# Kernel optimization log

Hardware: AMD Instinct MI355X
Metric: run time of the kernel (lower is better)

Reference implementation:

```python
import jax, jax.numpy as jnp
import numpy as np

DIM = 192
STATE = 64
B = 8
H = 64
W = 64
EPS_LN = 1e-5
EPS_BN = 1e-5


def _layernorm(x, g, b):
    m = jnp.mean(x, axis=-1, keepdims=True)
    v = jnp.mean((x - m) ** 2, axis=-1, keepdims=True)
    return (x - m) / jnp.sqrt(v + EPS_LN) * g + b


def _linear(x, w, b=None):
    # torch Linear convention: w is [out, in]
    y = jnp.einsum('...i,oi->...o', x, w)
    return y if b is None else y + b


def _parallel_scan(A, Bd, xp):
    # A, Bd, xp: [B, L, S]; h_t = A_t*h_{t-1} + Bd_t*xp_t via log-space cumsum
    A_safe = jnp.clip(A, 0.001, 0.999)
    log_A = jnp.log(A_safe + 1e-10)
    log_cum_A = jnp.cumsum(log_A, axis=1)
    log_cum_A_max = jnp.max(log_cum_A, axis=1, keepdims=True)
    cum_A = jnp.exp(log_cum_A - log_cum_A_max)
    BX = Bd * xp
    # prepend zeros, drop last: normalizer uses cumprod up to t-1
    log_pad = jnp.pad(log_cum_A - log_cum_A_max, ((0, 0), (1, 0), (0, 0)))[:, :-1]
    BX_norm = BX * jnp.exp(-log_pad)
    return jnp.cumsum(BX_norm, axis=1) * cum_A


def _ssm(x, ln_g, ln_b, xp_w, xp_b, dt_w, dt_b, A_log, B_w, C_w, Dp, out_w, out_b):
    xn = _layernorm(x, ln_g, ln_b)
    delta = jax.nn.softplus(_linear(xn, dt_w, dt_b)) * 0.01 + 0.0001  # [B,L,S]
    B_t = _linear(xn, B_w)
    C_t = _linear(xn, C_w)
    A = -jnp.exp(A_log)  # [S]
    x_proj = _linear(xn, xp_w, xp_b)
    deltaA = jnp.clip(delta * A, -10.0, -0.0001)
    A_disc = jnp.exp(deltaA)
    B_disc = delta * B_t
    h = _parallel_scan(A_disc, B_disc, x_proj)
    y = C_t * h
    y = jnp.where(jnp.all(jnp.isfinite(y)), y, jnp.zeros_like(y))
    y = _linear(y, out_w, out_b)
    return y + jnp.clip(Dp, -2.0, 2.0) * x


def reference(x, ln1_g, ln1_b, ln2_g, ln2_b, dw_w, bn_g, bn_b, bn_rm, bn_rv,
              ssm_ln_g, ssm_ln_b, xp_w, xp_b, dt_w, dt_b, A_log, B_w, C_w,
              D_param, out_w, out_b, mlp_w1, mlp_b1, mlp_w2, mlp_b2,
              alpha_local, alpha_ssm, alpha_mlp):
    identity = x
    # depthwise 3x3 conv + BatchNorm2d (eval mode, running stats)
    xc = jax.lax.conv_general_dilated(
        x, dw_w, (1, 1), 'SAME', feature_group_count=DIM,
        dimension_numbers=('NCHW', 'OIHW', 'NCHW'))
    scale = (bn_g / jnp.sqrt(bn_rv + EPS_BN))[None, :, None, None]
    x_local = (xc - bn_rm[None, :, None, None]) * scale + bn_b[None, :, None, None]
    # SSM branch on flattened spatial sequence
    x_seq = x.transpose(0, 2, 3, 1).reshape(B, H * W, DIM)
    x_seq = _layernorm(x_seq, ln1_g, ln1_b)
    x_seq = _ssm(x_seq, ssm_ln_g, ssm_ln_b, xp_w, xp_b, dt_w, dt_b, A_log,
                 B_w, C_w, D_param, out_w, out_b)
    x_ssm = x_seq.reshape(B, H, W, DIM).transpose(0, 3, 1, 2)
    xr = identity + alpha_local * x_local + alpha_ssm * x_ssm
    # residual MLP (dropout = identity at inference)
    x_mlp = xr.transpose(0, 2, 3, 1).reshape(B, H * W, DIM)
    x_mlp = _layernorm(x_mlp, ln2_g, ln2_b)
    x_mlp = _linear(jax.nn.gelu(_linear(x_mlp, mlp_w1, mlp_b1), approximate=False),
                    mlp_w2, mlp_b2)
    return xr + alpha_mlp * x_mlp.reshape(B, H, W, DIM).transpose(0, 3, 1, 2)


def setup_inputs() -> dict:
    key = jax.random.key(0)
    ks = jax.random.split(key, 12)
    def nrm(k, shape, s):
        return jax.random.normal(k, shape, jnp.float32) * s
    f32 = jnp.float32
    return {
        'x': jax.random.normal(ks[0], (B, DIM, H, W), f32),
        'ln1_g': jnp.ones(DIM, f32), 'ln1_b': jnp.zeros(DIM, f32),
        'ln2_g': jnp.ones(DIM, f32), 'ln2_b': jnp.zeros(DIM, f32),
        'dw_w': nrm(ks[1], (DIM, 1, 3, 3), 0.2),
        'bn_g': jnp.ones(DIM, f32), 'bn_b': jnp.zeros(DIM, f32),
        'bn_rm': jnp.zeros(DIM, f32), 'bn_rv': jnp.ones(DIM, f32),
        'ssm_ln_g': jnp.ones(DIM, f32), 'ssm_ln_b': jnp.zeros(DIM, f32),
        'xp_w': nrm(ks[2], (STATE, DIM), 0.05), 'xp_b': jnp.zeros(STATE, f32),
        'dt_w': nrm(ks[3], (STATE, DIM), 0.05), 'dt_b': jnp.zeros(STATE, f32),
        'A_log': jnp.log(jax.random.uniform(ks[4], (STATE,), f32) * 0.8 + 0.2),
        'B_w': nrm(ks[5], (STATE, DIM), 0.05),
        'C_w': nrm(ks[6], (STATE, DIM), 0.05),
        'D_param': jnp.zeros(DIM, f32),
        'out_w': nrm(ks[7], (DIM, STATE), 0.05), 'out_b': jnp.zeros(DIM, f32),
        'mlp_w1': nrm(ks[8], (4 * DIM, DIM), 0.03), 'mlp_b1': jnp.zeros(4 * DIM, f32),
        'mlp_w2': nrm(ks[9], (DIM, 4 * DIM), 0.03), 'mlp_b2': jnp.zeros(DIM, f32),
        'alpha_local': jnp.full((1,), 0.5, f32),
        'alpha_ssm': jnp.full((1,), 0.5, f32),
        'alpha_mlp': jnp.full((1,), 0.5, f32),
    }
```

## Files before the change

kernel.cpp:

```cpp
#include <hip/hip_runtime.h>
#include <hip/hip_bf16.h>
#include <math.h>


#define DEV static __device__ __forceinline__

constexpr int Bn = 8, Dm = 192, Ln = 4096, Sn = 64, Hd = 768;

typedef __attribute__((ext_vector_type(8))) short bf16x8;
typedef __attribute__((ext_vector_type(4))) float f32x4;

DEV float wave_sum(float v) {
#pragma unroll
  for (int off = 1; off < 64; off <<= 1) v += __shfl_xor(v, off);
  return v;
}

DEV short f2b(float x) {
  __hip_bfloat16 h = __float2bfloat16(x);
  return *(short*)&h;
}

DEV float b2f(short x) {
  __hip_bfloat16 h = *(__hip_bfloat16*)&x;
  return __bfloat162float(h);
}

__global__ __launch_bounds__(256) void k_ln(
    const float* __restrict__ x, const float* __restrict__ g1, const float* __restrict__ b1,
    const float* __restrict__ g2, const float* __restrict__ b2,
    short* __restrict__ xnb, short* __restrict__ xln1b) {
  __shared__ __align__(16) float tile[Dm * 65];
  int b = blockIdx.y, l0 = blockIdx.x * 64, tid = threadIdx.x;
  const float* xb = x + (size_t)b * Dm * Ln;
  for (int i = tid; i < Dm * 16; i += 256) {
    int d = i >> 4, l4 = (i & 15) << 2;
    float4 v = *(const float4*)&xb[d * Ln + l0 + l4];
    tile[d * 65 + l4]     = v.x; tile[d * 65 + l4 + 1] = v.y;
    tile[d * 65 + l4 + 2] = v.z; tile[d * 65 + l4 + 3] = v.w;
  }
  __syncthreads();
  int lane = tid & 63, wv = tid >> 6;
  float ga0 = g1[lane], ga1 = g1[lane + 64], ga2 = g1[lane + 128];
  float bb0 = b1[lane], bb1 = b1[lane + 64], bb2 = b1[lane + 128];
  float gc0 = g2[lane], gc1 = g2[lane + 64], gc2 = g2[lane + 128];
  float bc0 = b2[lane], bc1 = b2[lane + 64], bc2 = b2[lane + 128];
  for (int li = wv; li < 64; li += 4) {
    float v0 = tile[lane * 65 + li], v1 = tile[(lane + 64) * 65 + li], v2 = tile[(lane + 128) * 65 + li];
    float s  = wave_sum(v0 + v1 + v2);
    float sq = wave_sum(v0 * v0 + v1 * v1 + v2 * v2);
    float m = s * (1.f / 192.f);
    float inv = rsqrtf(sq * (1.f / 192.f) - m * m + 1e-5f);
    float y0 = (v0 - m) * inv * ga0 + bb0;
    float y1 = (v1 - m) * inv * ga1 + bb1;
    float y2 = (v2 - m) * inv * ga2 + bb2;
    float s2  = wave_sum(y0 + y1 + y2);
    float sq2 = wave_sum(y0 * y0 + y1 * y1 + y2 * y2);
    float m2 = s2 * (1.f / 192.f);
    float inv2 = rsqrtf(sq2 * (1.f / 192.f) - m2 * m2 + 1e-5f);
    size_t base = ((size_t)b * Ln + l0 + li) * Dm;
    xln1b[base + lane]       = f2b(y0);
    xln1b[base + lane + 64]  = f2b(y1);
    xln1b[base + lane + 128] = f2b(y2);
    xnb[base + lane]       = f2b((y0 - m2) * inv2 * gc0 + bc0);
    xnb[base + lane + 64]  = f2b((y1 - m2) * inv2 * gc1 + bc1);
    xnb[base + lane + 128] = f2b((y2 - m2) * inv2 * gc2 + bc2);
  }
}

__global__ __launch_bounds__(256) void k_wconv(
    const float* __restrict__ dt_w, const float* __restrict__ B_w,
    const float* __restrict__ C_w, const float* __restrict__ xp_w,
    const float* __restrict__ out_w, const float* __restrict__ w1,
    const float* __restrict__ w2, short* __restrict__ wb) {
  int i = blockIdx.x * 256 + threadIdx.x;
  const float4* src;
  if (i < 3072)       src = (const float4*)dt_w + i;
  else if (i < 6144)  src = (const float4*)B_w + (i - 3072);
  else if (i < 9216)  src = (const float4*)C_w + (i - 6144);
  else if (i < 12288) src = (const float4*)xp_w + (i - 9216);
  else if (i < 15360) src = (const float4*)out_w + (i - 12288);
  else if (i < 52224) src = (const float4*)w1 + (i - 15360);
  else                src = (const float4*)w2 + (i - 52224);
  float4 v = *src;
  int o = i * 4;
  wb[o]     = f2b(v.x); wb[o + 1] = f2b(v.y);
  wb[o + 2] = f2b(v.z); wb[o + 3] = f2b(v.w);
}

__global__ __launch_bounds__(256) void k_proj(
    const short* __restrict__ xnb, const short* __restrict__ wcat,
    const float* __restrict__ dt_b, const float* __restrict__ xp_b,
    const float* __restrict__ A_log, float* __restrict__ abc) {
  __shared__ __align__(16) short As[64 * 72];
  __shared__ __align__(16) short Bs[256 * 72];
  int m0 = blockIdx.x * 64, tid = threadIdx.x;
  int lane = tid & 63, l16 = lane & 15, quad = lane >> 4, w = tid >> 6;
  f32x4 acc[16] = {};
  for (int kt = 0; kt < 3; kt++) {
    int kb = kt * 64;
    for (int i = tid; i < 512; i += 256) {
      int row = i >> 3, c8 = (i & 7) * 8;
      *(float4*)&As[row * 72 + c8] = *(const float4*)&xnb[(size_t)(m0 + row) * 192 + kb + c8];
    }
    for (int i = tid; i < 2048; i += 256) {
      int row = i >> 3, c8 = (i & 7) * 8;
      *(float4*)&Bs[row * 72 + c8] = *(const float4*)&wcat[(size_t)row * 192 + kb + c8];
    }
    __syncthreads();
#pragma unroll
    for (int ks = 0; ks < 2; ks++) {
      int ko = ks * 32 + quad * 8;
      bf16x8 a0 = *(const bf16x8*)&As[(w * 16 + l16) * 72 + ko];
#pragma unroll
      for (int nh = 0; nh < 2; nh++) {
        bf16x8 bfr[8];
#pragma unroll
        for (int j = 0; j < 8; j++) bfr[j] = *(const bf16x8*)&Bs[((nh * 8 + j) * 16 + l16) * 72 + ko];
#pragma unroll
        for (int j = 0; j < 8; j++)
          acc[nh * 8 + j] = __builtin_amdgcn_mfma_f32_16x16x32_bf16(a0, bfr[j], acc[nh * 8 + j], 0, 0, 0);
      }
    }
    __syncthreads();
  }
  float Av[4], dtb[4], xpb[4];
#pragma unroll
  for (int ni = 0; ni < 4; ni++) {
    int s = ni * 16 + l16;
    Av[ni] = -expf(A_log[s]); dtb[ni] = dt_b[s]; xpb[ni] = xp_b[s];
  }
#pragma unroll
  for (int r = 0; r < 4; r++) {
    int m = m0 + w * 16 + quad * 4 + r;
    float* orow = abc + (size_t)m * 192;
#pragma unroll
    for (int ni = 0; ni < 4; ni++) {
      int s = ni * 16 + l16;
      float z = acc[ni][r] + dtb[ni];
      float sp = (z > 20.f) ? z : log1pf(expf(z));
      float delta = sp * 0.01f + 0.0001f;
      float bt  = acc[ni + 4][r];
      float ct  = acc[ni + 8][r];
      float xpv = acc[ni + 12][r] + xpb[ni];
      float dA = fminf(fmaxf(delta * Av[ni], -10.f), -0.0001f);
      float Ae = fminf(fmaxf(expf(dA), 0.001f), 0.999f) + 1e-10f;
      orow[s]       = Ae;
      orow[64 + s]  = delta * bt * xpv;
      orow[128 + s] = ct;
    }
  }
}

__global__ __launch_bounds__(64) void k_scan1(const float* __restrict__ abc, float* __restrict__ sums) {
  int c = blockIdx.x, b = blockIdx.y, s = threadIdx.x;
  const float* p = abc + ((size_t)b * Ln + c * 32) * 192;
  float prodA = 1.f, h = 0.f;
  int t = 0;
  if (c == 0) { prodA = p[s]; h = p[64 + s]; t = 1; }
#pragma unroll 4
  for (; t < 32; t++) {
    float a = p[t * 192 + s], bx = p[t * 192 + 64 + s];
    h = a * (h + bx);
    prodA *= a;
  }
  int ci = b * 128 + c;
  sums[(ci * 2 + 0) * 64 + s] = prodA;
  sums[(ci * 2 + 1) * 64 + s] = h;
}

__global__ __launch_bounds__(64) void k_scan2(const float* __restrict__ sums, float* __restrict__ carries) {
  int b = blockIdx.x, s = threadIdx.x;
  float cur = 0.f;
#pragma unroll 4
  for (int c = 0; c < 128; c++) {
    int ci = b * 128 + c;
    carries[ci * 64 + s] = cur;
    cur = sums[(ci * 2 + 0) * 64 + s] * cur + sums[(ci * 2 + 1) * 64 + s];
  }
}

__global__ __launch_bounds__(64) void k_scan3(const float* __restrict__ abc, const float* __restrict__ carries,
                                              short* __restrict__ y) {
  int c = blockIdx.x, b = blockIdx.y, s = threadIdx.x;
  size_t r0 = (size_t)b * Ln + c * 32;
  const float* p = abc + r0 * 192;
  short* yo = y + r0 * 64;
  float h = carries[(b * 128 + c) * 64 + s];
  int t = 0;
  if (c == 0) { h = p[64 + s]; yo[s] = f2b(p[128 + s] * h); t = 1; }
#pragma unroll 4
  for (; t < 32; t++) {
    float a = p[t * 192 + s], bx = p[t * 192 + 64 + s], ct = p[t * 192 + 128 + s];
    h = a * (h + bx);
    yo[t * 64 + s] = f2b(ct * h);
  }
}

__global__ __launch_bounds__(256) void k_out(
    const short* __restrict__ y, const short* __restrict__ owb, const float* __restrict__ out_b,
    const float* __restrict__ Dp, const short* __restrict__ xln1b, float* __restrict__ sout) {
  __shared__ __align__(16) short As[96 * 72];
  __shared__ __align__(16) short Bs[64 * 72];
  int l0g = blockIdx.x * 64, d0 = blockIdx.y * 96, tid = threadIdx.x;
  int lane = tid & 63, l16 = lane & 15, quad = lane >> 4;
  int wm = (tid >> 6) >> 1, wn = (tid >> 6) & 1;
  f32x4 acc[3][2] = {};
  for (int i = tid; i < 768; i += 256) {
    int row = i >> 3, c8 = (i & 7) * 8;
    *(float4*)&As[row * 72 + c8] = *(const float4*)&owb[(d0 + row) * 64 + c8];
  }
  for (int i = tid; i < 512; i += 256) {
    int row = i >> 3, c8 = (i & 7) * 8;
    *(float4*)&Bs[row * 72 + c8] = *(const float4*)&y[(size_t)(l0g + row) * 64 + c8];
  }
  __syncthreads();
#pragma unroll
  for (int ks = 0; ks < 2; ks++) {
    int ko = ks * 32 + quad * 8;
    bf16x8 a[3], b[2];
#pragma unroll
    for (int mi = 0; mi < 3; mi++) a[mi] = *(const bf16x8*)&As[(wm * 48 + mi * 16 + l16) * 72 + ko];
#pragma unroll
    for (int ni = 0; ni < 2; ni++) b[ni] = *(const bf16x8*)&Bs[(wn * 32 + ni * 16 + l16) * 72 + ko];
#pragma unroll
    for (int mi = 0; mi < 3; mi++)
#pragma unroll
      for (int ni = 0; ni < 2; ni++)
        acc[mi][ni] = __builtin_amdgcn_mfma_f32_16x16x32_bf16(a[mi], b[ni], acc[mi][ni], 0, 0, 0);
  }
  int bb = l0g >> 12;
#pragma unroll
  for (int mi = 0; mi < 3; mi++)
#pragma unroll
    for (int r = 0; r < 4; r++) {
      int d = d0 + wm * 48 + mi * 16 + quad * 4 + r;
      float ob = out_b[d];
      float dc = fminf(fmaxf(Dp[d], -2.f), 2.f);
#pragma unroll
      for (int ni = 0; ni < 2; ni++) {
        int l = l0g + wn * 32 + ni * 16 + l16;
        float v = acc[mi][ni][r] + ob;
        if (dc != 0.f) v += dc * b2f(xln1b[(size_t)l * 192 + d]);
        sout[((size_t)bb * Dm + d) * Ln + (l & 4095)] = v;
      }
    }
}

__global__ __launch_bounds__(256) void k_conv(
    const float* __restrict__ x, const float* __restrict__ dw,
    const float* __restrict__ bn_g, const float* __restrict__ bn_b,
    const float* __restrict__ bn_rm, const float* __restrict__ bn_rv,
    const float* __restrict__ sout, const float* __restrict__ a_loc,
    const float* __restrict__ a_ssm, float* __restrict__ xr) {
  __shared__ __align__(16) float xs[64 * 64];
  int d = blockIdx.x, b = blockIdx.y, tid = threadIdx.x;
  const float* xp = x + ((size_t)b * Dm + d) * Ln;
  for (int i = tid; i < 1024; i += 256) ((float4*)xs)[i] = ((const float4*)xp)[i];
  __syncthreads();
  float w[9];
#pragma unroll
  for (int k = 0; k < 9; k++) w[k] = dw[d * 9 + k];
  float scale = bn_g[d] * rsqrtf(bn_rv[d] + 1e-5f);
  float rm = bn_rm[d], bb = bn_b[d];
  float al = a_loc[0], as_ = a_ssm[0];
  const float* sp = sout + ((size_t)b * Dm + d) * Ln;
  float* xo = xr + ((size_t)b * Dm + d) * Ln;
  for (int i = tid; i < 4096; i += 256) {
    int h = i >> 6, wc = i & 63;
    float acc = 0.f;
#pragma unroll
    for (int kh = 0; kh < 3; kh++) {
      int hh = h + kh - 1;
      if (hh < 0 || hh >= 64) continue;
#pragma unroll
      for (int kw = 0; kw < 3; kw++) {
        int ww2 = wc + kw - 1;
        if (ww2 < 0 || ww2 >= 64) continue;
        acc += xs[hh * 64 + ww2] * w[kh * 3 + kw];
      }
    }
    float xl = (acc - rm) * scale + bb;
    xo[i] = xs[i] + al * xl + as_ * sp[i];
  }
}

__global__ __launch_bounds__(256) void k_ln2(
    const float* __restrict__ xr, const float* __restrict__ g, const float* __restrict__ bb,
    short* __restrict__ xn2) {
  __shared__ __align__(16) float tile[Dm * 65];
  int b = blockIdx.y, l0 = blockIdx.x * 64, tid = threadIdx.x;
  const float* xb = xr + (size_t)b * Dm * Ln;
  for (int i = tid; i < Dm * 16; i += 256) {
    int d = i >> 4, l4 = (i & 15) << 2;
    float4 v = *(const float4*)&xb[d * Ln + l0 + l4];
    tile[d * 65 + l4]     = v.x; tile[d * 65 + l4 + 1] = v.y;
    tile[d * 65 + l4 + 2] = v.z; tile[d * 65 + l4 + 3] = v.w;
  }
  __syncthreads();
  int lane = tid & 63, wv = tid >> 6;
  float g0 = g[lane], g1v = g[lane + 64], g2v = g[lane + 128];
  float b0 = bb[lane], b1v = bb[lane + 64], b2v = bb[lane + 128];
  for (int li = wv; li < 64; li += 4) {
    float v0 = tile[lane * 65 + li], v1 = tile[(lane + 64) * 65 + li], v2 = tile[(lane + 128) * 65 + li];
    float s  = wave_sum(v0 + v1 + v2);
    float sq = wave_sum(v0 * v0 + v1 * v1 + v2 * v2);
    float m = s * (1.f / 192.f);
    float inv = rsqrtf(sq * (1.f / 192.f) - m * m + 1e-5f);
    size_t base = ((size_t)b * Ln + l0 + li) * Dm;
    xn2[base + lane]       = f2b((v0 - m) * inv * g0 + b0);
    xn2[base + lane + 64]  = f2b((v1 - m) * inv * g1v + b1v);
    xn2[base + lane + 128] = f2b((v2 - m) * inv * g2v + b2v);
  }
}

__global__ __launch_bounds__(256) void k_gemm1(
    const short* __restrict__ xn2, const short* __restrict__ w1b,
    const float* __restrict__ b1h, short* __restrict__ hid) {
  __shared__ __align__(16) short smem[2 * 128 * 88];
  short* As = smem;
  short* Bs = smem + 128 * 88;
  int m0 = blockIdx.x * 128, n0 = blockIdx.y * 128, tid = threadIdx.x;
  int lane = tid & 63, l16 = lane & 15, quad = lane >> 4;
  int wm = (tid >> 6) >> 1, wn = (tid >> 6) & 1;
  f32x4 acc[4][4] = {};
  for (int kt = 0; kt < 3; kt++) {
    int kb = kt * 64;
    for (int i = tid; i < 1024; i += 256) {
      int row = i >> 3, c8 = (i & 7) * 8;
      *(float4*)&As[row * 88 + c8] = *(const float4*)&xn2[(size_t)(m0 + row) * 192 + kb + c8];
      *(float4*)&Bs[row * 88 + c8] = *(const float4*)&w1b[(size_t)(n0 + row) * 192 + kb + c8];
    }
    __syncthreads();
#pragma unroll
    for (int ks = 0; ks < 2; ks++) {
      int ko = ks * 32 + quad * 8;
      bf16x8 a[4], b[4];
#pragma unroll
      for (int mi = 0; mi < 4; mi++) a[mi] = *(const bf16x8*)&As[(wm * 64 + mi * 16 + l16) * 88 + ko];
#pragma unroll
      for (int ni = 0; ni < 4; ni++) b[ni] = *(const bf16x8*)&Bs[(wn * 64 + ni * 16 + l16) * 88 + ko];
#pragma unroll
      for (int mi = 0; mi < 4; mi++)
#pragma unroll
        for (int ni = 0; ni < 4; ni++)
          acc[mi][ni] = __builtin_amdgcn_mfma_f32_16x16x32_bf16(a[mi], b[ni], acc[mi][ni], 0, 0, 0);
    }
    __syncthreads();
  }
  short* Cs = smem;
  float bias4[4];
#pragma unroll
  for (int ni = 0; ni < 4; ni++) bias4[ni] = b1h[n0 + wn * 64 + ni * 16 + l16];
#pragma unroll
  for (int mi = 0; mi < 4; mi++)
#pragma unroll
    for (int ni = 0; ni < 4; ni++) {
      int n = wn * 64 + ni * 16 + l16;
#pragma unroll
      for (int r = 0; r < 4; r++) {
        int m = wm * 64 + mi * 16 + quad * 4 + r;
        float v = acc[mi][ni][r] + bias4[ni];
        float g = 0.5f * v * (1.f + erff(v * 0.70710678118f));
        Cs[m * 136 + n] = f2b(g);
      }
    }
  __syncthreads();
  for (int i = tid; i < 2048; i += 256) {
    int m = i >> 4, ch = i & 15;
    *(float4*)&hid[(size_t)(m0 + m) * 768 + n0 + ch * 8] = *(const float4*)&Cs[m * 136 + ch * 8];
  }
}

__global__ __launch_bounds__(256) void k_gemm2(
    const short* __restrict__ hid, const short* __restrict__ w2b,
    const float* __restrict__ b2o, const float* __restrict__ xr,
    const float* __restrict__ am, float* __restrict__ out) {
  __shared__ __align__(16) short Wt[96 * 88];
  __shared__ __align__(16) short Ht[64 * 88];
  int l0g = blockIdx.x * 64, d0 = blockIdx.y * 96, tid = threadIdx.x;
  int lane = tid & 63, l16 = lane & 15, quad = lane >> 4;
  int wm = (tid >> 6) >> 1, wn = (tid >> 6) & 1;
  f32x4 acc[3][2] = {};
  for (int kt = 0; kt < 12; kt++) {
    int kb = kt * 64;
    for (int i = tid; i < 768; i += 256) {
      int row = i >> 3, c8 = (i & 7) * 8;
      *(float4*)&Wt[row * 88 + c8] = *(const float4*)&w2b[(size_t)(d0 + row) * 768 + kb + c8];
    }
    for (int i = tid; i < 512; i += 256) {
      int row = i >> 3, c8 = (i & 7) * 8;
      *(float4*)&Ht[row * 88 + c8] = *(const float4*)&hid[(size_t)(l0g + row) * 768 + kb + c8];
    }
    __syncthreads();
#pragma unroll
    for (int ks = 0; ks < 2; ks++) {
      int ko = ks * 32 + quad * 8;
      bf16x8 a[3], b[2];
#pragma unroll
      for (int mi = 0; mi < 3; mi++) a[mi] = *(const bf16x8*)&Wt[(wm * 48 + mi * 16 + l16) * 88 + ko];
#pragma unroll
      for (int ni = 0; ni < 2; ni++) b[ni] = *(const bf16x8*)&Ht[(wn * 32 + ni * 16 + l16) * 88 + ko];
#pragma unroll
      for (int mi = 0; mi < 3; mi++)
#pragma unroll
        for (int ni = 0; ni < 2; ni++)
          acc[mi][ni] = __builtin_amdgcn_mfma_f32_16x16x32_bf16(a[mi], b[ni], acc[mi][ni], 0, 0, 0);
    }
    __syncthreads();
  }
  float alpha = am[0];
#pragma unroll
  for (int mi = 0; mi < 3; mi++)
#pragma unroll
    for (int r = 0; r < 4; r++) {
      int d = d0 + wm * 48 + mi * 16 + quad * 4 + r;
      float bias = b2o[d];
#pragma unroll
      for (int ni = 0; ni < 2; ni++) {
        int lg = l0g + wn * 32 + ni * 16 + l16;
        size_t idx = ((size_t)(lg >> 12) * Dm + d) * Ln + (lg & 4095);
        out[idx] = xr[idx] + alpha * (acc[mi][ni][r] + bias);
      }
    }
}

extern "C" void kernel_launch(void* const* d_in, const int* in_sizes, int n_in,
                              void* d_out, int out_size, void* d_ws, size_t ws_size,
                              hipStream_t stream) {
  (void)in_sizes; (void)n_in; (void)out_size; (void)ws_size;
  const float* x     = (const float*)d_in[0];
  const float* ln1_g = (const float*)d_in[1];
  const float* ln1_b = (const float*)d_in[2];
  const float* ln2_g = (const float*)d_in[3];
  const float* ln2_b = (const float*)d_in[4];
  const float* dw_w  = (const float*)d_in[5];
  const float* bn_g  = (const float*)d_in[6];
  const float* bn_b  = (const float*)d_in[7];
  const float* bn_rm = (const float*)d_in[8];
  const float* bn_rv = (const float*)d_in[9];
  const float* ssm_g = (const float*)d_in[10];
  const float* ssm_b = (const float*)d_in[11];
  const float* xp_w  = (const float*)d_in[12];
  const float* xp_b  = (const float*)d_in[13];
  const float* dt_w  = (const float*)d_in[14];
  const float* dt_b  = (const float*)d_in[15];
  const float* A_log = (const float*)d_in[16];
  const float* B_w   = (const float*)d_in[17];
  const float* C_w   = (const float*)d_in[18];
  const float* Dp    = (const float*)d_in[19];
  const float* out_w = (const float*)d_in[20];
  const float* out_b = (const float*)d_in[21];
  const float* w1    = (const float*)d_in[22];
  const float* b1    = (const float*)d_in[23];
  const float* w2    = (const float*)d_in[24];
  const float* b2    = (const float*)d_in[25];
  const float* a_loc = (const float*)d_in[26];
  const float* a_ssm = (const float*)d_in[27];
  const float* a_mlp = (const float*)d_in[28];

  float* ws = (float*)d_ws;
  short* xnb   = (short*)ws;
  short* xln1b = (short*)(ws + 3145728);
  float* abc   = ws + 6291456;
  short* yB    = (short*)(ws + 12582912);
  float* sout  = ws + 13729792;
  float* xr    = ws + 20021248;
  short* wb    = (short*)(ws + 26312704);
  float* sums  = ws + 26490880;
  float* carr  = ws + 26621952;
  short* wcatb = wb;
  short* owb   = wb + 49152;
  short* w1b   = wb + 61440;
  short* w2b   = wb + 208896;
  short* xn2   = (short*)ws;
  short* hid   = (short*)(ws + 6291456);
  float* out   = (float*)d_out;

  k_ln   <<<dim3(64, 8),  256, 0, stream>>>(x, ln1_g, ln1_b, ssm_g, ssm_b, xnb, xln1b);
  k_wconv<<<dim3(348),    256, 0, stream>>>(dt_w, B_w, C_w, xp_w, out_w, w1, w2, wb);
  k_proj <<<dim3(512),    256, 0, stream>>>(xnb, wcatb, dt_b, xp_b, A_log, abc);
  k_scan1<<<dim3(128, 8),  64, 0, stream>>>(abc, sums);
  k_scan2<<<dim3(8),       64, 0, stream>>>(sums, carr);
  k_scan3<<<dim3(128, 8),  64, 0, stream>>>(abc, carr, yB);
  k_out  <<<dim3(512, 2), 256, 0, stream>>>(yB, owb, out_b, Dp, xln1b, sout);
  k_conv <<<dim3(192, 8), 256, 0, stream>>>(x, dw_w, bn_g, bn_b, bn_rm, bn_rv, sout, a_loc, a_ssm, xr);
  k_ln2  <<<dim3(64, 8),  256, 0, stream>>>(xr, ln2_g, ln2_b, xn2);
  k_gemm1<<<dim3(256, 6), 256, 0, stream>>>(xn2, w1b, b1, hid);
  k_gemm2<<<dim3(512, 2), 256, 0, stream>>>(hid, w2b, b2, xr, a_mlp, out);
}
```

Before: 294.8 us.

## Split and compress scan intermediates, halve LN tiles, read activations directly in GEMMs

Measured after the change: 309.1 us. 1.05x slower.

```diff
diff --git a/kernel.cpp b/kernel.cpp
--- a/kernel.cpp
+++ b/kernel.cpp
@@ -30,14 +30,14 @@
     const float* __restrict__ x, const float* __restrict__ g1, const float* __restrict__ b1,
     const float* __restrict__ g2, const float* __restrict__ b2,
     short* __restrict__ xnb, short* __restrict__ xln1b) {
-  __shared__ __align__(16) float tile[Dm * 65];
-  int b = blockIdx.y, l0 = blockIdx.x * 64, tid = threadIdx.x;
+  __shared__ __align__(16) float tile[Dm * 33];
+  int b = blockIdx.y, l0 = blockIdx.x * 32, tid = threadIdx.x;
   const float* xb = x + (size_t)b * Dm * Ln;
-  for (int i = tid; i < Dm * 16; i += 256) {
-    int d = i >> 4, l4 = (i & 15) << 2;
+  for (int i = tid; i < Dm * 8; i += 256) {
+    int d = i >> 3, l4 = (i & 7) << 2;
     float4 v = *(const float4*)&xb[d * Ln + l0 + l4];
-    tile[d * 65 + l4]     = v.x; tile[d * 65 + l4 + 1] = v.y;
-    tile[d * 65 + l4 + 2] = v.z; tile[d * 65 + l4 + 3] = v.w;
+    tile[d * 33 + l4]     = v.x; tile[d * 33 + l4 + 1] = v.y;
+    tile[d * 33 + l4 + 2] = v.z; tile[d * 33 + l4 + 3] = v.w;
   }
   __syncthreads();
   int lane = tid & 63, wv = tid >> 6;
@@ -45,8 +45,8 @@
   float bb0 = b1[lane], bb1 = b1[lane + 64], bb2 = b1[lane + 128];
   float gc0 = g2[lane], gc1 = g2[lane + 64], gc2 = g2[lane + 128];
   float bc0 = b2[lane], bc1 = b2[lane + 64], bc2 = b2[lane + 128];
-  for (int li = wv; li < 64; li += 4) {
-    float v0 = tile[lane * 65 + li], v1 = tile[(lane + 64) * 65 + li], v2 = tile[(lane + 128) * 65 + li];
+  for (int li = wv; li < 32; li += 4) {
+    float v0 = tile[lane * 33 + li], v1 = tile[(lane + 64) * 33 + li], v2 = tile[(lane + 128) * 33 + li];
     float s  = wave_sum(v0 + v1 + v2);
     float sq = wave_sum(v0 * v0 + v1 * v1 + v2 * v2);
     float m = s * (1.f / 192.f);
@@ -74,97 +74,102 @@
     const float* __restrict__ out_w, const float* __restrict__ w1,
     const float* __restrict__ w2, short* __restrict__ wb) {
   int i = blockIdx.x * 256 + threadIdx.x;
+  if (i >= 89088) return;
+  if (i < 12288) {
+    int mat = i / 3072, rem = i % 3072;
+    int s = rem / 48, c4 = rem % 48;
+    const float4* src = (mat == 0) ? (const float4*)dt_w
+                      : (mat == 1) ? (const float4*)B_w
+                      : (mat == 2) ? (const float4*)C_w : (const float4*)xp_w;
+    float4 v = src[rem];
+    int r = (s >> 5) * 128 + (mat * 2 + ((s >> 4) & 1)) * 16 + (s & 15);
+    int o = r * 192 + c4 * 4;
+    wb[o] = f2b(v.x); wb[o + 1] = f2b(v.y); wb[o + 2] = f2b(v.z); wb[o + 3] = f2b(v.w);
+    return;
+  }
   const float4* src;
-  if (i < 3072)       src = (const float4*)dt_w + i;
-  else if (i < 6144)  src = (const float4*)B_w + (i - 3072);
-  else if (i < 9216)  src = (const float4*)C_w + (i - 6144);
-  else if (i < 12288) src = (const float4*)xp_w + (i - 9216);
-  else if (i < 15360) src = (const float4*)out_w + (i - 12288);
+  if (i < 15360)      src = (const float4*)out_w + (i - 12288);
   else if (i < 52224) src = (const float4*)w1 + (i - 15360);
   else                src = (const float4*)w2 + (i - 52224);
   float4 v = *src;
   int o = i * 4;
-  wb[o]     = f2b(v.x); wb[o + 1] = f2b(v.y);
-  wb[o + 2] = f2b(v.z); wb[o + 3] = f2b(v.w);
+  wb[o] = f2b(v.x); wb[o + 1] = f2b(v.y); wb[o + 2] = f2b(v.z); wb[o + 3] = f2b(v.w);
 }
 
 __global__ __launch_bounds__(256) void k_proj(
     const short* __restrict__ xnb, const short* __restrict__ wcat,
     const float* __restrict__ dt_b, const float* __restrict__ xp_b,
-    const float* __restrict__ A_log, float* __restrict__ abc) {
-  __shared__ __align__(16) short As[64 * 72];
+    const float* __restrict__ A_log, float* __restrict__ aA, unsigned* __restrict__ bxc) {
   __shared__ __align__(16) short Bs[256 * 72];
-  int m0 = blockIdx.x * 64, tid = threadIdx.x;
-  int lane = tid & 63, l16 = lane & 15, quad = lane >> 4, w = tid >> 6;
-  f32x4 acc[16] = {};
+  int m0 = blockIdx.x * 32, tid = threadIdx.x;
+  int lane = tid & 63, l16 = lane & 15, quad = lane >> 4;
+  int wm = (tid >> 6) >> 1, wn = (tid >> 6) & 1;
+  f32x4 acc[8] = {};
   for (int kt = 0; kt < 3; kt++) {
     int kb = kt * 64;
-    for (int i = tid; i < 512; i += 256) {
-      int row = i >> 3, c8 = (i & 7) * 8;
-      *(float4*)&As[row * 72 + c8] = *(const float4*)&xnb[(size_t)(m0 + row) * 192 + kb + c8];
-    }
     for (int i = tid; i < 2048; i += 256) {
       int row = i >> 3, c8 = (i & 7) * 8;
-      *(float4*)&Bs[row * 72 + c8] = *(const float4*)&wcat[(size_t)row * 192 + kb + c8];
+      *(float4*)&Bs[row * 72 + c8] = *(const float4*)&wcat[row * 192 + kb + c8];
     }
     __syncthreads();
 #pragma unroll
     for (int ks = 0; ks < 2; ks++) {
       int ko = ks * 32 + quad * 8;
-      bf16x8 a0 = *(const bf16x8*)&As[(w * 16 + l16) * 72 + ko];
-#pragma unroll
-      for (int nh = 0; nh < 2; nh++) {
-        bf16x8 bfr[8];
-#pragma unroll
-        for (int j = 0; j < 8; j++) bfr[j] = *(const bf16x8*)&Bs[((nh * 8 + j) * 16 + l16) * 72 + ko];
-#pragma unroll
-        for (int j = 0; j < 8; j++)
-          acc[nh * 8 + j] = __builtin_amdgcn_mfma_f32_16x16x32_bf16(a0, bfr[j], acc[nh * 8 + j], 0, 0, 0);
+      bf16x8 a0 = *(const bf16x8*)&xnb[(size_t)(m0 + wm * 16 + l16) * 192 + kb + ko];
+#pragma unroll
+      for (int j = 0; j < 8; j++) {
+        bf16x8 bf = *(const bf16x8*)&Bs[(wn * 128 + j * 16 + l16) * 72 + ko];
+        acc[j] = __builtin_amdgcn_mfma_f32_16x16x32_bf16(a0, bf, acc[j], 0, 0, 0);
       }
     }
     __syncthreads();
   }
-  float Av[4], dtb[4], xpb[4];
-#pragma unroll
-  for (int ni = 0; ni < 4; ni++) {
-    int s = ni * 16 + l16;
-    Av[ni] = -expf(A_log[s]); dtb[ni] = dt_b[s]; xpb[ni] = xp_b[s];
+  float Av[2], dtbv[2], xpbv[2];
+#pragma unroll
+  for (int sub = 0; sub < 2; sub++) {
+    int s = wn * 32 + sub * 16 + l16;
+    Av[sub] = -expf(A_log[s]); dtbv[sub] = dt_b[s]; xpbv[sub] = xp_b[s];
   }
 #pragma unroll
   for (int r = 0; r < 4; r++) {
-    int m = m0 + w * 16 + quad * 4 + r;
-    float* orow = abc + (size_t)m * 192;
-#pragma unroll
-    for (int ni = 0; ni < 4; ni++) {
-      int s = ni * 16 + l16;
-      float z = acc[ni][r] + dtb[ni];
+    int m = m0 + wm * 16 + quad * 4 + r;
+#pragma unroll
+    for (int sub = 0; sub < 2; sub++) {
+      int s = wn * 32 + sub * 16 + l16;
+      float z = acc[0 + sub][r] + dtbv[sub];
       float sp = (z > 20.f) ? z : log1pf(expf(z));
       float delta = sp * 0.01f + 0.0001f;
-      float bt  = acc[ni + 4][r];
-      float ct  = acc[ni + 8][r];
-      float xpv = acc[ni + 12][r] + xpb[ni];
-      float dA = fminf(fmaxf(delta * Av[ni], -10.f), -0.0001f);
+      float bt  = acc[2 + sub][r];
+      float ct  = acc[4 + sub][r];
+      float xpv = acc[6 + sub][r] + xpbv[sub];
+      float dA = fminf(fmaxf(delta * Av[sub], -10.f), -0.0001f);
       float Ae = fminf(fmaxf(expf(dA), 0.001f), 0.999f) + 1e-10f;
-      orow[s]       = Ae;
-      orow[64 + s]  = delta * bt * xpv;
-      orow[128 + s] = ct;
-    }
-  }
-}
-
-__global__ __launch_bounds__(64) void k_scan1(const float* __restrict__ abc, float* __restrict__ sums) {
+      aA[(size_t)m * 64 + s] = Ae;
+      unsigned pk = (unsigned)(unsigned short)f2b(delta * bt * xpv)
+                  | ((unsigned)(unsigned short)f2b(ct) << 16);
+      bxc[(size_t)m * 64 + s] = pk;
+    }
+  }
+}
+
+__global__ __launch_bounds__(64) void k_scan1(const float* __restrict__ aA,
+                                              const unsigned* __restrict__ bxc,
+                                              float* __restrict__ sums) {
   int c = blockIdx.x, b = blockIdx.y, s = threadIdx.x;
-  const float* p = abc + ((size_t)b * Ln + c * 32) * 192;
+  size_t r0 = (size_t)b * Ln + c * 16;
+  const float* ap = aA + r0 * 64;
+  const unsigned* bp = bxc + r0 * 64;
   float prodA = 1.f, h = 0.f;
   int t = 0;
-  if (c == 0) { prodA = p[s]; h = p[64 + s]; t = 1; }
+  if (c == 0) { prodA = ap[s]; h = b2f((short)(bp[s] & 0xFFFF)); t = 1; }
 #pragma unroll 4
-  for (; t < 32; t++) {
-    float a = p[t * 192 + s], bx = p[t * 192 + 64 + s];
+  for (; t < 16; t++) {
+    float a = ap[t * 64 + s];
+    float bx = b2f((short)(bp[t * 64 + s] & 0xFFFF));
     h = a * (h + bx);
     prodA *= a;
   }
-  int ci = b * 128 + c;
+  int ci = b * 256 + c;
   sums[(ci * 2 + 0) * 64 + s] = prodA;
   sums[(ci * 2 + 1) * 64 + s] = h;
 }
@@ -173,27 +178,36 @@
   int b = blockIdx.x, s = threadIdx.x;
   float cur = 0.f;
 #pragma unroll 4
-  for (int c = 0; c < 128; c++) {
-    int ci = b * 128 + c;
+  for (int c = 0; c < 256; c++) {
+    int ci = b * 256 + c;
     carries[ci * 64 + s] = cur;
     cur = sums[(ci * 2 + 0) * 64 + s] * cur + sums[(ci * 2 + 1) * 64 + s];
   }
 }
 
-__global__ __launch_bounds__(64) void k_scan3(const float* __restrict__ abc, const float* __restrict__ carries,
+__global__ __launch_bounds__(64) void k_scan3(const float* __restrict__ aA,
+                                              const unsigned* __restrict__ bxc,
+                                              const float* __restrict__ carries,
                                               short* __restrict__ y) {
   int c = blockIdx.x, b = blockIdx.y, s = threadIdx.x;
-  size_t r0 = (size_t)b * Ln + c * 32;
-  const float* p = abc + r0 * 192;
+  size_t r0 = (size_t)b * Ln + c * 16;
+  const float* ap = aA + r0 * 64;
+  const unsigned* bp = bxc + r0 * 64;
   short* yo = y + r0 * 64;
-  float h = carries[(b * 128 + c) * 64 + s];
+  float h = carries[(b * 256 + c) * 64 + s];
   int t = 0;
-  if (c == 0) { h = p[64 + s]; yo[s] = f2b(p[128 + s] * h); t = 1; }
+  if (c == 0) {
+    unsigned u = bp[s];
+    h = b2f((short)(u & 0xFFFF));
+    yo[s] = f2b(b2f((short)(u >> 16)) * h);
+    t = 1;
+  }
 #pragma unroll 4
-  for (; t < 32; t++) {
-    float a = p[t * 192 + s], bx = p[t * 192 + 64 + s], ct = p[t * 192 + 128 + s];
-    h = a * (h + bx);
-    yo[t * 64 + s] = f2b(ct * h);
+  for (; t < 16; t++) {
+    unsigned u = bp[t * 64 + s];
+    float a = ap[t * 64 + s];
+    h = a * (h + b2f((short)(u & 0xFFFF)));
+    yo[t * 64 + s] = f2b(b2f((short)(u >> 16)) * h);
   }
 }
 
@@ -201,7 +215,6 @@
     const short* __restrict__ y, const short* __restrict__ owb, const float* __restrict__ out_b,
     const float* __restrict__ Dp, const short* __restrict__ xln1b, float* __restrict__ sout) {
   __shared__ __align__(16) short As[96 * 72];
-  __shared__ __align__(16) short Bs[64 * 72];
   int l0g = blockIdx.x * 64, d0 = blockIdx.y * 96, tid = threadIdx.x;
   int lane = tid & 63, l16 = lane & 15, quad = lane >> 4;
   int wm = (tid >> 6) >> 1, wn = (tid >> 6) & 1;
@@ -210,10 +223,6 @@
     int row = i >> 3, c8 = (i & 7) * 8;
     *(float4*)&As[row * 72 + c8] = *(const float4*)&owb[(d0 + row) * 64 + c8];
   }
-  for (int i = tid; i < 512; i += 256) {
-    int row = i >> 3, c8 = (i & 7) * 8;
-    *(float4*)&Bs[row * 72 + c8] = *(const float4*)&y[(size_t)(l0g + row) * 64 + c8];
-  }
   __syncthreads();
 #pragma unroll
   for (int ks = 0; ks < 2; ks++) {
@@ -222,7 +231,8 @@
 #pragma unroll
     for (int mi = 0; mi < 3; mi++) a[mi] = *(const bf16x8*)&As[(wm * 48 + mi * 16 + l16) * 72 + ko];
 #pragma unroll
-    for (int ni = 0; ni < 2; ni++) b[ni] = *(const bf16x8*)&Bs[(wn * 32 + ni * 16 + l16) * 72 + ko];
+    for (int ni = 0; ni < 2; ni++)
+      b[ni] = *(const bf16x8*)&y[(size_t)(l0g + wn * 32 + ni * 16 + l16) * 64 + ko];
 #pragma unroll
     for (int mi = 0; mi < 3; mi++)
 #pragma unroll
@@ -288,21 +298,21 @@
 __global__ __launch_bounds__(256) void k_ln2(
     const float* __restrict__ xr, const float* __restrict__ g, const float* __restrict__ bb,
     short* __restrict__ xn2) {
-  __shared__ __align__(16) float tile[Dm * 65];
-  int b = blockIdx.y, l0 = blockIdx.x * 64, tid = threadIdx.x;
+  __shared__ __align__(16) float tile[Dm * 33];
+  int b = blockIdx.y, l0 = blockIdx.x * 32, tid = threadIdx.x;
   const float* xb = xr + (size_t)b * Dm * Ln;
-  for (int i = tid; i < Dm * 16; i += 256) {
-    int d = i >> 4, l4 = (i & 15) << 2;
+  for (int i = tid; i < Dm * 8; i += 256) {
+    int d = i >> 3, l4 = (i & 7) << 2;
     float4 v = *(const float4*)&xb[d * Ln + l0 + l4];
-    tile[d * 65 + l4]     = v.x; tile[d * 65 + l4 + 1] = v.y;
-    tile[d * 65 + l4 + 2] = v.z; tile[d * 65 + l4 + 3] = v.w;
+    tile[d * 33 + l4]     = v.x; tile[d * 33 + l4 + 1] = v.y;
+    tile[d * 33 + l4 + 2] = v.z; tile[d * 33 + l4 + 3] = v.w;
   }
   __syncthreads();
   int lane = tid & 63, wv = tid >> 6;
   float g0 = g[lane], g1v = g[lane + 64], g2v = g[lane + 128];
   float b0 = bb[lane], b1v = bb[lane + 64], b2v = bb[lane + 128];
-  for (int li = wv; li < 64; li += 4) {
-    float v0 = tile[lane * 65 + li], v1 = tile[(lane + 64) * 65 + li], v2 = tile[(lane + 128) * 65 + li];
+  for (int li = wv; li < 32; li += 4) {
+    float v0 = tile[lane * 33 + li], v1 = tile[(lane + 64) * 33 + li], v2 = tile[(lane + 128) * 33 + li];
     float s  = wave_sum(v0 + v1 + v2);
     float sq = wave_sum(v0 * v0 + v1 * v1 + v2 * v2);
     float m = s * (1.f / 192.f);
@@ -317,9 +327,8 @@
 __global__ __launch_bounds__(256) void k_gemm1(
     const short* __restrict__ xn2, const short* __restrict__ w1b,
     const float* __restrict__ b1h, short* __restrict__ hid) {
-  __shared__ __align__(16) short smem[2 * 128 * 88];
-  short* As = smem;
-  short* Bs = smem + 128 * 88;
+  __shared__ __align__(16) short smem[128 * 136];
+  short* Bs = smem;
   int m0 = blockIdx.x * 128, n0 = blockIdx.y * 128, tid = threadIdx.x;
   int lane = tid & 63, l16 = lane & 15, quad = lane >> 4;
   int wm = (tid >> 6) >> 1, wn = (tid >> 6) & 1;
@@ -328,8 +337,7 @@
     int kb = kt * 64;
     for (int i = tid; i < 1024; i += 256) {
       int row = i >> 3, c8 = (i & 7) * 8;
-      *(float4*)&As[row * 88 + c8] = *(const float4*)&xn2[(size_t)(m0 + row) * 192 + kb + c8];
-      *(float4*)&Bs[row * 88 + c8] = *(const float4*)&w1b[(size_t)(n0 + row) * 192 + kb + c8];
+      *(float4*)&Bs[row * 72 + c8] = *(const float4*)&w1b[(size_t)(n0 + row) * 192 + kb + c8];
     }
     __syncthreads();
 #pragma unroll
@@ -337,9 +345,10 @@
       int ko = ks * 32 + quad * 8;
       bf16x8 a[4], b[4];
 #pragma unroll
-      for (int mi = 0; mi < 4; mi++) a[mi] = *(const bf16x8*)&As[(wm * 64 + mi * 16 + l16) * 88 + ko];
-#pragma unroll
-      for (int ni = 0; ni < 4; ni++) b[ni] = *(const bf16x8*)&Bs[(wn * 64 + ni * 16 + l16) * 88 + ko];
+      for (int mi = 0; mi < 4; mi++)
+        a[mi] = *(const bf16x8*)&xn2[(size_t)(m0 + wm * 64 + mi * 16 + l16) * 192 + kb + ko];
+#pragma unroll
+      for (int ni = 0; ni < 4; ni++) b[ni] = *(const bf16x8*)&Bs[(wn * 64 + ni * 16 + l16) * 72 + ko];
 #pragma unroll
       for (int mi = 0; mi < 4; mi++)
 #pragma unroll
@@ -376,8 +385,7 @@
     const short* __restrict__ hid, const short* __restrict__ w2b,
     const float* __restrict__ b2o, const float* __restrict__ xr,
     const float* __restrict__ am, float* __restrict__ out) {
-  __shared__ __align__(16) short Wt[96 * 88];
-  __shared__ __align__(16) short Ht[64 * 88];
+  __shared__ __align__(16) short Wt[96 * 72];
   int l0g = blockIdx.x * 64, d0 = blockIdx.y * 96, tid = threadIdx.x;
   int lane = tid & 63, l16 = lane & 15, quad = lane >> 4;
   int wm = (tid >> 6) >> 1, wn = (tid >> 6) & 1;
@@ -386,11 +394,7 @@
     int kb = kt * 64;
     for (int i = tid; i < 768; i += 256) {
       int row = i >> 3, c8 = (i & 7) * 8;
-      *(float4*)&Wt[row * 88 + c8] = *(const float4*)&w2b[(size_t)(d0 + row) * 768 + kb + c8];
-    }
-    for (int i = tid; i < 512; i += 256) {
-      int row = i >> 3, c8 = (i & 7) * 8;
-      *(float4*)&Ht[row * 88 + c8] = *(const float4*)&hid[(size_t)(l0g + row) * 768 + kb + c8];
+      *(float4*)&Wt[row * 72 + c8] = *(const float4*)&w2b[(size_t)(d0 + row) * 768 + kb + c8];
     }
     __syncthreads();
 #pragma unroll
@@ -398,9 +402,10 @@
       int ko = ks * 32 + quad * 8;
       bf16x8 a[3], b[2];
 #pragma unroll
-      for (int mi = 0; mi < 3; mi++) a[mi] = *(const bf16x8*)&Wt[(wm * 48 + mi * 16 + l16) * 88 + ko];
-#pragma unroll
-      for (int ni = 0; ni < 2; ni++) b[ni] = *(const bf16x8*)&Ht[(wn * 32 + ni * 16 + l16) * 88 + ko];
+      for (int mi = 0; mi < 3; mi++) a[mi] = *(const bf16x8*)&Wt[(wm * 48 + mi * 16 + l16) * 72 + ko];
+#pragma unroll
+      for (int ni = 0; ni < 2; ni++)
+        b[ni] = *(const bf16x8*)&hid[(size_t)(l0g + wn * 32 + ni * 16 + l16) * 768 + kb + ko];
 #pragma unroll
       for (int mi = 0; mi < 3; mi++)
 #pragma unroll
@@ -460,32 +465,33 @@
   const float* a_mlp = (const float*)d_in[28];
 
   float* ws = (float*)d_ws;
-  short* xnb   = (short*)ws;
-  short* xln1b = (short*)(ws + 3145728);
-  float* abc   = ws + 6291456;
-  short* yB    = (short*)(ws + 12582912);
-  float* sout  = ws + 13729792;
-  float* xr    = ws + 20021248;
-  short* wb    = (short*)(ws + 26312704);
-  float* sums  = ws + 26490880;
-  float* carr  = ws + 26621952;
-  short* wcatb = wb;
-  short* owb   = wb + 49152;
-  short* w1b   = wb + 61440;
-  short* w2b   = wb + 208896;
-  short* xn2   = (short*)ws;
-  short* hid   = (short*)(ws + 6291456);
-  float* out   = (float*)d_out;
-
-  k_ln   <<<dim3(64, 8),  256, 0, stream>>>(x, ln1_g, ln1_b, ssm_g, ssm_b, xnb, xln1b);
+  short*    xnb   = (short*)ws;
+  short*    xln1b = (short*)(ws + 3145728);
+  float*    aA    = ws + 6291456;
+  unsigned* bxc   = (unsigned*)(ws + 8388608);
+  short*    yB    = (short*)(ws + 10485760);
+  float*    sout  = ws + 11534336;
+  float*    xr    = ws + 17825792;
+  short*    wb    = (short*)(ws + 24117248);
+  float*    sums  = ws + 24295424;
+  float*    carr  = ws + 24557568;
+  short*    hid   = (short*)(ws + 24688640);
+  short*    xn2   = (short*)(ws + 37271552);
+  short*    wcatb = wb;
+  short*    owb   = wb + 49152;
+  short*    w1b   = wb + 61440;
+  short*    w2b   = wb + 208896;
+  float*    out   = (float*)d_out;
+
+  k_ln   <<<dim3(128, 8), 256, 0, stream>>>(x, ln1_g, ln1_b, ssm_g, ssm_b, xnb, xln1b);
   k_wconv<<<dim3(348),    256, 0, stream>>>(dt_w, B_w, C_w, xp_w, out_w, w1, w2, wb);
-  k_proj <<<dim3(512),    256, 0, stream>>>(xnb, wcatb, dt_b, xp_b, A_log, abc);
-  k_scan1<<<dim3(128, 8),  64, 0, stream>>>(abc, sums);
+  k_proj <<<dim3(1024),   256, 0, stream>>>(xnb, wcatb, dt_b, xp_b, A_log, aA, bxc);
+  k_scan1<<<dim3(256, 8),  64, 0, stream>>>(aA, bxc, sums);
   k_scan2<<<dim3(8),       64, 0, stream>>>(sums, carr);
-  k_scan3<<<dim3(128, 8),  64, 0, stream>>>(abc, carr, yB);
+  k_scan3<<<dim3(256, 8),  64, 0, stream>>>(aA, bxc, carr, yB);
   k_out  <<<dim3(512, 2), 256, 0, stream>>>(yB, owb, out_b, Dp, xln1b, sout);
   k_conv <<<dim3(192, 8), 256, 0, stream>>>(x, dw_w, bn_g, bn_b, bn_rm, bn_rv, sout, a_loc, a_ssm, xr);
-  k_ln2  <<<dim3(64, 8),  256, 0, stream>>>(xr, ln2_g, ln2_b, xn2);
+  k_ln2  <<<dim3(128, 8), 256, 0, stream>>>(xr, ln2_g, ln2_b, xn2);
   k_gemm1<<<dim3(256, 6), 256, 0, stream>>>(xn2, w1b, b1, hid);
   k_gemm2<<<dim3(512, 2), 256, 0, stream>>>(hid, w2b, b2, xr, a_mlp, out);
 }
```
